# Kernel tuning notes

Measured on AMD Instinct MI355X. Metric: run time of the kernel, lower is better.

The kernel has to match this reference:

```python
import jax, jax.numpy as jnp
import numpy as np

NX, NY, NT = 128, 128, 64          # global space-time grid
LX, LY = 2.0, 2.0                  # periodic domain extents
K_NB = 128                         # neighbors per query
NHEAD = 4
EPS = 1e-5


def setup_inputs() -> dict:
    key = jax.random.key(0)
    ks = jax.random.split(key, 12)
    N = NX * NY * NT
    B, d, dff, L = 2048, 64, 128, 2
    nrm = lambda k, s: jax.random.normal(k, s, jnp.float32) * 0.05
    return {
        "q_lin_idx": jax.random.randint(ks[0], (B,), 0, N),
        "offsets_ijk": jax.random.randint(ks[1], (K_NB, 3), 0, 8),
        "coords": jax.random.uniform(ks[2], (N, 3), jnp.float32) * 2.0,
        "vals": jax.random.normal(ks[3], (N, 3), jnp.float32),
        "log_gammas": jnp.zeros((3,), jnp.float32),
        "proj_w": nrm(ks[4], (d, 6)), "proj_b": jnp.zeros((d,), jnp.float32),
        "qkv_w": nrm(ks[5], (L, 3 * d, d)), "qkv_b": jnp.zeros((L, 3 * d), jnp.float32),
        "out_w": nrm(ks[6], (L, d, d)), "out_b": jnp.zeros((L, d), jnp.float32),
        "ln1_s": jnp.ones((L, d), jnp.float32), "ln1_b": jnp.zeros((L, d), jnp.float32),
        "ff1_w": nrm(ks[7], (L, dff, d)), "ff1_b": jnp.zeros((L, dff), jnp.float32),
        "ff2_w": nrm(ks[8], (L, d, dff)), "ff2_b": jnp.zeros((L, d), jnp.float32),
        "ln2_s": jnp.ones((L, d), jnp.float32), "ln2_b": jnp.zeros((L, d), jnp.float32),
        "head_ln_s": jnp.ones((d,), jnp.float32), "head_ln_b": jnp.zeros((d,), jnp.float32),
        "head1_w": nrm(ks[9], (d, d)), "head1_b": jnp.zeros((d,), jnp.float32),
        "head2_w": nrm(ks[10], (3, d)), "head2_b": jnp.zeros((3,), jnp.float32),
    }


def _ln(x, s, b):
    m = x.mean(-1, keepdims=True)
    v = ((x - m) ** 2).mean(-1, keepdims=True)
    return (x - m) * jax.lax.rsqrt(v + EPS) * s + b


def _dper(a, b, L):
    # periodic relative delta in [-L/2, L/2)
    return (a - b + 0.5 * L) % L - 0.5 * L


def reference(q_lin_idx, offsets_ijk, coords, vals, log_gammas, proj_w, proj_b,
              qkv_w, qkv_b, out_w, out_b, ln1_s, ln1_b, ff1_w, ff1_b, ff2_w, ff2_b,
              ln2_s, ln2_b, head_ln_s, head_ln_b, head1_w, head1_b, head2_w, head2_b):
    # --- periodic-wrapped neighbor indices (div/mod on linear index) ---
    i = q_lin_idx // (NY * NT)
    r = q_lin_idx % (NY * NT)
    j = r // NT
    kk = r % NT
    di, dj, dk = offsets_ijk[:, 0], offsets_ijk[:, 1], offsets_ijk[:, 2]
    I = (i[:, None] + di[None, :]) % NX          # wrap_x
    J = (j[:, None] + dj[None, :]) % NY          # wrap_y
    T = jnp.clip(kk[:, None] + dk[None, :], 0, NT - 1)  # no wrap in t
    nb = I * (NY * NT) + J * NT + T              # [B, K]

    # --- gather + relative-delta encode ---
    q_xyz = coords[q_lin_idx]                    # [B, 3]
    nb_xyz = coords[nb]                          # [B, K, 3]
    dx = _dper(nb_xyz[..., 0], q_xyz[:, None, 0], LX)
    dy = _dper(nb_xyz[..., 1], q_xyz[:, None, 1], LY)
    dt = nb_xyz[..., 2] - q_xyz[:, None, 2]
    rel = jnp.stack([dx, dy, dt], -1) * jnp.exp(log_gammas)[None, None, :]
    tokens = jnp.concatenate([rel, vals[nb]], -1)  # [B, K, 6]

    # --- input projection + TransformerEncoder (post-norm, relu FF) ---
    h = tokens @ proj_w.T + proj_b               # [B, S, d]
    B, S, d = h.shape
    dh = d // NHEAD
    scale = 1.0 / np.sqrt(dh).astype(np.float32)
    for l in range(qkv_w.shape[0]):
        qkv = h @ qkv_w[l].T + qkv_b[l]
        qh, kh, vh = jnp.split(qkv, 3, axis=-1)
        qh = qh.reshape(B, S, NHEAD, dh).transpose(0, 2, 1, 3)
        kh = kh.reshape(B, S, NHEAD, dh).transpose(0, 2, 1, 3)
        vh = vh.reshape(B, S, NHEAD, dh).transpose(0, 2, 1, 3)
        att = jax.nn.softmax(jnp.einsum('bhqd,bhkd->bhqk', qh, kh) * scale, axis=-1)
        o = jnp.einsum('bhqk,bhkd->bhqd', att, vh).transpose(0, 2, 1, 3).reshape(B, S, d)
        h = _ln(h + (o @ out_w[l].T + out_b[l]), ln1_s[l], ln1_b[l])
        ff = jax.nn.relu(h @ ff1_w[l].T + ff1_b[l]) @ ff2_w[l].T + ff2_b[l]
        h = _ln(h + ff, ln2_s[l], ln2_b[l])

    # --- mean pool over neighbors + head ---
    hm = h.mean(axis=1)                          # [B, d]
    g = _ln(hm, head_ln_s, head_ln_b)
    g = jax.nn.gelu(g @ head1_w.T + head1_b, approximate=False)
    return g @ head2_w.T + head2_b               # [B, 3]
```

## Files before the change

### kernel.cpp

```cpp
#include <hip/hip_runtime.h>
#include <math.h>

#define NXg 128
#define NYg 128
#define NTg 64
#define SEQ 128
#define DIM 64
#define NH 4
#define DHd 16
#define DFFd 128
#define NLAYER 2
#define EPSf 1e-5f

typedef _Float16 f16x8 __attribute__((ext_vector_type(8)));
typedef _Float16 f16x4 __attribute__((ext_vector_type(4)));
typedef __fp16 fp16x2 __attribute__((ext_vector_type(2)));
typedef float f32x4 __attribute__((ext_vector_type(4)));

#define MFMA16(a, b, c) __builtin_amdgcn_mfma_f32_16x16x32_f16(a, b, c, 0, 0, 0)

union FragU { int d[4]; f16x8 v; };
union H4U  { int d[2]; f16x4 v; };
union P2U  { int i; fp16x2 h; };

__device__ __forceinline__ int pk2(float a, float b) {
  P2U u;
  u.h = __builtin_amdgcn_cvt_pkrtz(a, b);
  return u.i;
}
__device__ __forceinline__ float2 up2(int p) {
  P2U u; u.i = p;
  return make_float2((float)u.h[0], (float)u.h[1]);
}

__device__ __forceinline__ f16x8 zero8() {
  f16x8 z;
#pragma unroll
  for (int i = 0; i < 8; ++i) z[i] = (_Float16)0.0f;
  return z;
}
__device__ __forceinline__ f32x4 zero4f() {
  f32x4 z;
  z[0] = 0.f; z[1] = 0.f; z[2] = 0.f; z[3] = 0.f;
  return z;
}
__device__ __forceinline__ f16x8 ld8(const _Float16* p) { return *(const f16x8*)p; }

__device__ __forceinline__ f16x8 frag_k16p(int p0, int p1, int quad, int l15) {
  int slA = ((2 * quad) * 16 + l15) & 63;
  int slB = ((2 * quad + 1) * 16 + l15) & 63;
  FragU u;
  u.d[0] = __shfl(p0, slA, 64);
  u.d[1] = __shfl(p1, slA, 64);
  u.d[2] = __shfl(p0, slB, 64);
  u.d[3] = __shfl(p1, slB, 64);
  if (quad >= 2) { u.d[0] = 0; u.d[1] = 0; u.d[2] = 0; u.d[3] = 0; }
  return u.v;
}

__device__ __forceinline__ f16x8 frag_k64(const int* pk, int kt, int quad, int l15) {
  const int slA = (2 * (quad & 1)) * 16 + l15;
  const int slB = (2 * (quad & 1) + 1) * 16 + l15;
  const bool hi = quad >= 2;
  int a0 = __shfl(pk[4 * kt + 0], slA, 64), b0 = __shfl(pk[4 * kt + 2], slA, 64);
  int a1 = __shfl(pk[4 * kt + 1], slA, 64), b1 = __shfl(pk[4 * kt + 3], slA, 64);
  int a2 = __shfl(pk[4 * kt + 0], slB, 64), b2 = __shfl(pk[4 * kt + 2], slB, 64);
  int a3 = __shfl(pk[4 * kt + 1], slB, 64), b3 = __shfl(pk[4 * kt + 3], slB, 64);
  FragU u;
  u.d[0] = hi ? b0 : a0;
  u.d[1] = hi ? b1 : a1;
  u.d[2] = hi ? b2 : a2;
  u.d[3] = hi ? b3 : a3;
  return u.v;
}

__device__ __forceinline__ void res_ln_qt(const f32x4 acc[4], int pkX[8],
                                          const float* __restrict__ bias,
                                          const float* __restrict__ lns,
                                          const float* __restrict__ lnb,
                                          int quad) {
  float v[4][4];
  float s = 0.f;
#pragma unroll
  for (int mt = 0; mt < 4; ++mt) {
    f32x4 bb = *(const f32x4*)(bias + mt * 16 + quad * 4);
    float2 x0 = up2(pkX[mt * 2 + 0]);
    float2 x1 = up2(pkX[mt * 2 + 1]);
    v[mt][0] = acc[mt][0] + bb[0] + x0.x;
    v[mt][1] = acc[mt][1] + bb[1] + x0.y;
    v[mt][2] = acc[mt][2] + bb[2] + x1.x;
    v[mt][3] = acc[mt][3] + bb[3] + x1.y;
    s += (v[mt][0] + v[mt][1]) + (v[mt][2] + v[mt][3]);
  }
  s += __shfl_xor(s, 16, 64);
  s += __shfl_xor(s, 32, 64);
  const float mu = s * (1.0f / 64.0f);
  float q2 = 0.f;
#pragma unroll
  for (int mt = 0; mt < 4; ++mt)
#pragma unroll
    for (int jr = 0; jr < 4; ++jr) { float d = v[mt][jr] - mu; q2 = fmaf(d, d, q2); }
  q2 += __shfl_xor(q2, 16, 64);
  q2 += __shfl_xor(q2, 32, 64);
  const float rstd = rsqrtf(q2 * (1.0f / 64.0f) + EPSf);
#pragma unroll
  for (int mt = 0; mt < 4; ++mt) {
    f32x4 sv = *(const f32x4*)(lns + mt * 16 + quad * 4);
    f32x4 bv = *(const f32x4*)(lnb + mt * 16 + quad * 4);
    float o0 = fmaf((v[mt][0] - mu) * rstd, sv[0], bv[0]);
    float o1 = fmaf((v[mt][1] - mu) * rstd, sv[1], bv[1]);
    float o2 = fmaf((v[mt][2] - mu) * rstd, sv[2], bv[2]);
    float o3 = fmaf((v[mt][3] - mu) * rstd, sv[3], bv[3]);
    pkX[mt * 2 + 0] = pk2(o0, o1);
    pkX[mt * 2 + 1] = pk2(o2, o3);
  }
}

__global__ void prep_weights(const float* __restrict__ qkv_w,
                             const float* __restrict__ out_w,
                             const float* __restrict__ ff1_w,
                             const float* __restrict__ ff2_w,
                             _Float16* __restrict__ wsH) {
  int i = blockIdx.x * 256 + threadIdx.x;
  if (i < 24576) wsH[i] = (_Float16)qkv_w[i];
  else if (i < 32768) wsH[i] = (_Float16)out_w[i - 24576];
  else if (i < 49152) wsH[i] = (_Float16)ff1_w[i - 32768];
  else if (i < 65536) wsH[i] = (_Float16)ff2_w[i - 49152];
}

__global__ __launch_bounds__(256, 3)
void fieldformer_mfma(const int* __restrict__ q_lin_idx,
                      const int* __restrict__ offsets_ijk,
                      const float* __restrict__ coords,
                      const float* __restrict__ vals,
                      const float* __restrict__ log_gammas,
                      const float* __restrict__ proj_w,
                      const float* __restrict__ proj_b,
                      const float* __restrict__ qkv_b,
                      const float* __restrict__ out_b,
                      const float* __restrict__ ln1_s,
                      const float* __restrict__ ln1_b,
                      const float* __restrict__ ff1_b,
                      const float* __restrict__ ff2_b,
                      const float* __restrict__ ln2_s,
                      const float* __restrict__ ln2_b,
                      const float* __restrict__ head_ln_s,
                      const float* __restrict__ head_ln_b,
                      const float* __restrict__ head1_w,
                      const float* __restrict__ head1_b,
                      const float* __restrict__ head2_w,
                      const float* __restrict__ head2_b,
                      const _Float16* __restrict__ wH,
                      float* __restrict__ out) {
  __shared__ __align__(16) _Float16 sK[128 * 72];
  __shared__ __align__(16) _Float16 sV[64 * 136];

  const int tid = threadIdx.x;
  const int wv = tid >> 6;
  const int lane = tid & 63;
  const int quad = lane >> 4;
  const int l15 = lane & 15;
  const int b = blockIdx.x;

  {
    const int row = tid >> 1, hf = tid & 1;
    const int q = q_lin_idx[b];
    const int qi = q / (NYg * NTg);
    const int qrem = q - qi * (NYg * NTg);
    const int qj = qrem / NTg;
    const int qk = qrem - qj * NTg;
    const int di = offsets_ijk[row * 3 + 0];
    const int dj = offsets_ijk[row * 3 + 1];
    const int dk = offsets_ijk[row * 3 + 2];
    const int I = (qi + di) % NXg;
    const int J = (qj + dj) % NYg;
    int T = qk + dk; T = T < 0 ? 0 : (T > NTg - 1 ? NTg - 1 : T);
    const int nb = I * (NYg * NTg) + J * NTg + T;
    const float qx = coords[q * 3 + 0], qy = coords[q * 3 + 1], qz = coords[q * 3 + 2];
    const float nx_ = coords[nb * 3 + 0], ny_ = coords[nb * 3 + 1], nz_ = coords[nb * 3 + 2];
    float ax = nx_ - qx + 1.0f; ax -= 2.0f * floorf(ax * 0.5f); ax -= 1.0f;
    float ay = ny_ - qy + 1.0f; ay -= 2.0f * floorf(ay * 0.5f); ay -= 1.0f;
    const float at = nz_ - qz;
    float tok[6];
    tok[0] = ax * expf(log_gammas[0]);
    tok[1] = ay * expf(log_gammas[1]);
    tok[2] = at * expf(log_gammas[2]);
    tok[3] = vals[nb * 3 + 0];
    tok[4] = vals[nb * 3 + 1];
    tok[5] = vals[nb * 3 + 2];
#pragma unroll
    for (int ci = 0; ci < 32; ++ci) {
      const int c = hf * 32 + ci;
      const float* w = proj_w + c * 6;
      float a = proj_b[c];
      a = fmaf(tok[0], w[0], a); a = fmaf(tok[1], w[1], a);
      a = fmaf(tok[2], w[2], a); a = fmaf(tok[3], w[3], a);
      a = fmaf(tok[4], w[4], a); a = fmaf(tok[5], w[5], a);
      sK[row * 72 + c] = (_Float16)a;
    }
  }
  __syncthreads();

  int pkX[2][8];
#pragma unroll
  for (int qt = 0; qt < 2; ++qt) {
    const int q = (wv * 2 + qt) * 16 + l15;
#pragma unroll
    for (int mt = 0; mt < 4; ++mt) {
      int2 t = *(const int2*)(sK + q * 72 + mt * 16 + quad * 4);
      pkX[qt][mt * 2 + 0] = t.x;
      pkX[qt][mt * 2 + 1] = t.y;
    }
  }

  for (int l = 0; l < NLAYER; ++l) {
    const _Float16* qkvH = wH + l * 192 * 64;
    const _Float16* woutH = wH + 24576 + l * 64 * 64;
    const _Float16* ff1H = wH + 32768 + l * 128 * 64;
    const _Float16* ff2H = wH + 49152 + l * 64 * 128;
    const float* bqkv = qkv_b + l * 192;

    __syncthreads();

    int pkQ[2][8];
    {
      f16x8 bxf[2][2];
#pragma unroll
      for (int qt = 0; qt < 2; ++qt)
#pragma unroll
        for (int kt = 0; kt < 2; ++kt) bxf[qt][kt] = frag_k64(pkX[qt], kt, quad, l15);
#pragma unroll
      for (int hd = 0; hd < NH; ++hd) {
        f32x4 dq[2] = {zero4f(), zero4f()};
        f32x4 dk[2] = {zero4f(), zero4f()};
        f32x4 dv[2] = {zero4f(), zero4f()};
#pragma unroll
        for (int kt = 0; kt < 2; ++kt) {
          f16x8 awq = ld8(qkvH + (hd * 16 + l15) * 64 + kt * 32 + quad * 8);
          f16x8 awk = ld8(qkvH + (64 + hd * 16 + l15) * 64 + kt * 32 + quad * 8);
          f16x8 awv = ld8(qkvH + (128 + hd * 16 + l15) * 64 + kt * 32 + quad * 8);
#pragma unroll
          for (int qt = 0; qt < 2; ++qt) {
            dq[qt] = MFMA16(awq, bxf[qt][kt], dq[qt]);
            dk[qt] = MFMA16(awk, bxf[qt][kt], dk[qt]);
            dv[qt] = MFMA16(awv, bxf[qt][kt], dv[qt]);
          }
        }
        const f32x4 bq4 = *(const f32x4*)(bqkv + hd * 16 + quad * 4);
        const f32x4 bk4 = *(const f32x4*)(bqkv + 64 + hd * 16 + quad * 4);
        const f32x4 bv4 = *(const f32x4*)(bqkv + 128 + hd * 16 + quad * 4);
#pragma unroll
        for (int qt = 0; qt < 2; ++qt) {
          const int q = (wv * 2 + qt) * 16 + l15;
          H4U k4;
          k4.d[0] = pk2(dk[qt][0] + bk4[0], dk[qt][1] + bk4[1]);
          k4.d[1] = pk2(dk[qt][2] + bk4[2], dk[qt][3] + bk4[3]);
          *(f16x4*)(sK + q * 72 + hd * 16 + quad * 4) = k4.v;
#pragma unroll
          for (int jr = 0; jr < 4; ++jr)
            sV[(hd * 16 + quad * 4 + jr) * 136 + q] = (_Float16)(dv[qt][jr] + bv4[jr]);
          pkQ[qt][hd * 2 + 0] = pk2((dq[qt][0] + bq4[0]) * 0.25f, (dq[qt][1] + bq4[1]) * 0.25f);
          pkQ[qt][hd * 2 + 1] = pk2((dq[qt][2] + bq4[2]) * 0.25f, (dq[qt][3] + bq4[3]) * 0.25f);
        }
      }
    }
    __syncthreads();

    int pkO[2][8];
#pragma unroll
    for (int hd = 0; hd < NH; ++hd) {
#pragma unroll
      for (int qt = 0; qt < 2; ++qt) {
        f16x8 bqf = frag_k16p(pkQ[qt][hd * 2 + 0], pkQ[qt][hd * 2 + 1], quad, l15);
        float s0 = 0.f;
        f32x4 ov = zero4f();
#pragma unroll
        for (int kt2 = 0; kt2 < 4; ++kt2) {
          int pkP[4];
#pragma unroll
          for (int mi = 0; mi < 2; ++mi) {
            const int mt = kt2 * 2 + mi;
            f16x8 ak = (quad < 2) ? ld8(sK + (mt * 16 + l15) * 72 + hd * 16 + quad * 8)
                                  : zero8();
            f32x4 zc = zero4f();
            f32x4 sc = MFMA16(ak, bqf, zc);
            float e0 = __expf(sc[0]), e1 = __expf(sc[1]);
            float e2 = __expf(sc[2]), e3 = __expf(sc[3]);
            s0 += (e0 + e1) + (e2 + e3);
            pkP[mi * 2 + 0] = pk2(e0, e1);
            pkP[mi * 2 + 1] = pk2(e2, e3);
          }
          f16x8 av = ld8(sV + (hd * 16 + l15) * 136 + kt2 * 32 + quad * 8);
          f16x8 bp = frag_k64(pkP, 0, quad, l15);
          ov = MFMA16(av, bp, ov);
        }
        s0 += __shfl_xor(s0, 16, 64);
        s0 += __shfl_xor(s0, 32, 64);
        const float inv = 1.0f / s0;
        pkO[qt][hd * 2 + 0] = pk2(ov[0] * inv, ov[1] * inv);
        pkO[qt][hd * 2 + 1] = pk2(ov[2] * inv, ov[3] * inv);
      }
    }

#pragma unroll
    for (int qt = 0; qt < 2; ++qt) {
      f32x4 y2[4] = {zero4f(), zero4f(), zero4f(), zero4f()};
#pragma unroll
      for (int kt = 0; kt < 2; ++kt) {
        f16x8 bof = frag_k64(pkO[qt], kt, quad, l15);
#pragma unroll
        for (int mt = 0; mt < 4; ++mt) {
          f16x8 aw = ld8(woutH + (mt * 16 + l15) * 64 + kt * 32 + quad * 8);
          y2[mt] = MFMA16(aw, bof, y2[mt]);
        }
      }
      res_ln_qt(y2, pkX[qt], out_b + l * 64, ln1_s + l * 64, ln1_b + l * 64, quad);
    }

#pragma unroll
    for (int qt = 0; qt < 2; ++qt) {
      f16x8 bx2[2];
#pragma unroll
      for (int kt = 0; kt < 2; ++kt) bx2[kt] = frag_k64(pkX[qt], kt, quad, l15);
      const float* b1 = ff1_b + l * 128;
      f32x4 g4[4] = {zero4f(), zero4f(), zero4f(), zero4f()};
#pragma unroll
      for (int kt = 0; kt < 4; ++kt) {
        int pkH[4];
#pragma unroll
        for (int mi = 0; mi < 2; ++mi) {
          const int mt = kt * 2 + mi;
          f32x4 f8 = zero4f();
#pragma unroll
          for (int k2 = 0; k2 < 2; ++k2) {
            f16x8 aw = ld8(ff1H + (mt * 16 + l15) * 64 + k2 * 32 + quad * 8);
            f8 = MFMA16(aw, bx2[k2], f8);
          }
          f32x4 bb = *(const f32x4*)(b1 + mt * 16 + quad * 4);
          pkH[mi * 2 + 0] = pk2(fmaxf(f8[0] + bb[0], 0.f), fmaxf(f8[1] + bb[1], 0.f));
          pkH[mi * 2 + 1] = pk2(fmaxf(f8[2] + bb[2], 0.f), fmaxf(f8[3] + bb[3], 0.f));
        }
        f16x8 bh = frag_k64(pkH, 0, quad, l15);
#pragma unroll
        for (int mt2 = 0; mt2 < 4; ++mt2) {
          f16x8 aw = ld8(ff2H + (mt2 * 16 + l15) * 128 + kt * 32 + quad * 8);
          g4[mt2] = MFMA16(aw, bh, g4[mt2]);
        }
      }
      res_ln_qt(g4, pkX[qt], ff2_b + l * 64, ln2_s + l * 64, ln2_b + l * 64, quad);
    }
  }

  __syncthreads();
  {
    float* pf = (float*)sK;
    float* gsc = pf + 256;
    float* asc = gsc + 64;
    f32x4 cs[4];
#pragma unroll
    for (int mt = 0; mt < 4; ++mt) {
      float2 a0 = up2(pkX[0][mt * 2 + 0]), a1 = up2(pkX[0][mt * 2 + 1]);
      float2 b0 = up2(pkX[1][mt * 2 + 0]), b1 = up2(pkX[1][mt * 2 + 1]);
      cs[mt][0] = a0.x + b0.x;
      cs[mt][1] = a0.y + b0.y;
      cs[mt][2] = a1.x + b1.x;
      cs[mt][3] = a1.y + b1.y;
    }
#pragma unroll
    for (int d = 1; d <= 8; d <<= 1)
#pragma unroll
      for (int mt = 0; mt < 4; ++mt)
#pragma unroll
        for (int jr = 0; jr < 4; ++jr) cs[mt][jr] += __shfl_xor(cs[mt][jr], d, 64);
    if (l15 == 0) {
#pragma unroll
      for (int mt = 0; mt < 4; ++mt)
        *(f32x4*)(pf + wv * 64 + mt * 16 + quad * 4) = cs[mt];
    }
    __syncthreads();
    if (tid < 64) {
      const float hm = (pf[tid] + pf[64 + tid] + pf[128 + tid] + pf[192 + tid]) * (1.0f / 128.0f);
      float t = hm;
      t += __shfl_xor(t, 1, 64);  t += __shfl_xor(t, 2, 64);
      t += __shfl_xor(t, 4, 64);  t += __shfl_xor(t, 8, 64);
      t += __shfl_xor(t, 16, 64); t += __shfl_xor(t, 32, 64);
      const float mu = t * (1.0f / 64.0f);
      const float dv = hm - mu;
      float v2 = dv * dv;
      v2 += __shfl_xor(v2, 1, 64);  v2 += __shfl_xor(v2, 2, 64);
      v2 += __shfl_xor(v2, 4, 64);  v2 += __shfl_xor(v2, 8, 64);
      v2 += __shfl_xor(v2, 16, 64); v2 += __shfl_xor(v2, 32, 64);
      const float var = v2 * (1.0f / 64.0f);
      gsc[tid] = fmaf(dv * rsqrtf(var + EPSf), head_ln_s[tid], head_ln_b[tid]);
    }
    __syncthreads();
    if (tid < 64) {
      float z = head1_b[tid];
      for (int k = 0; k < 64; ++k) z = fmaf(gsc[k], head1_w[tid * 64 + k], z);
      asc[tid] = 0.5f * z * (1.0f + erff(z * 0.70710678118654752f));
    }
    __syncthreads();
    if (tid < 3) {
      float z = head2_b[tid];
      for (int k = 0; k < 64; ++k) z = fmaf(asc[k], head2_w[tid * 64 + k], z);
      out[b * 3 + tid] = z;
    }
  }
}

extern "C" void kernel_launch(void* const* d_in, const int* in_sizes, int n_in,
                              void* d_out, int out_size, void* d_ws, size_t ws_size,
                              hipStream_t stream) {
  (void)n_in; (void)ws_size; (void)out_size;
  const int B = in_sizes[0];
  _Float16* wsH = (_Float16*)d_ws;

  prep_weights<<<dim3(256), dim3(256), 0, stream>>>(
      (const float*)d_in[7],
      (const float*)d_in[9],
      (const float*)d_in[13],
      (const float*)d_in[15],
      wsH);

  fieldformer_mfma<<<dim3(B), dim3(256), 0, stream>>>(
      (const int*)d_in[0],
      (const int*)d_in[1],
      (const float*)d_in[2],
      (const float*)d_in[3],
      (const float*)d_in[4],
      (const float*)d_in[5],
      (const float*)d_in[6],
      (const float*)d_in[8],
      (const float*)d_in[10],
      (const float*)d_in[11],
      (const float*)d_in[12],
      (const float*)d_in[14],
      (const float*)d_in[16],
      (const float*)d_in[17],
      (const float*)d_in[18],
      (const float*)d_in[19],
      (const float*)d_in[20],
      (const float*)d_in[21],
      (const float*)d_in[22],
      (const float*)d_in[23],
      (const float*)d_in[24],
      wsH,
      (float*)d_out);
}
```

Baseline: 319.7 us.

## Use 512 threads per block with one 16-token tile per wave

Doubles the block to 8 waves so that each wave handles a single 16-row query tile instead of two, and the token projection is split four ways per row. This removes the per-wave qt loop, which cuts register pressure and raises the number of waves available to hide MFMA and LDS latency. The cost is that each wave now loads the shared weight fragments for only one tile, so weight-load reuse across tiles drops, and the final reduction sums over 8 per-wave partials.

```diff
diff --git a/kernel.cpp b/kernel.cpp
--- a/kernel.cpp
+++ b/kernel.cpp
@@ -128,7 +128,7 @@
   else if (i < 65536) wsH[i] = (_Float16)ff2_w[i - 49152];
 }
 
-__global__ __launch_bounds__(256, 3)
+__global__ __launch_bounds__(512, 4)
 void fieldformer_mfma(const int* __restrict__ q_lin_idx,
                       const int* __restrict__ offsets_ijk,
                       const float* __restrict__ coords,
@@ -161,12 +161,13 @@
   const int quad = lane >> 4;
   const int l15 = lane & 15;
   const int b = blockIdx.x;
+  const int q = wv * 16 + l15;
 
   {
-    const int row = tid >> 1, hf = tid & 1;
-    const int q = q_lin_idx[b];
-    const int qi = q / (NYg * NTg);
-    const int qrem = q - qi * (NYg * NTg);
+    const int row = tid >> 2, part = tid & 3;
+    const int qq = q_lin_idx[b];
+    const int qi = qq / (NYg * NTg);
+    const int qrem = qq - qi * (NYg * NTg);
     const int qj = qrem / NTg;
     const int qk = qrem - qj * NTg;
     const int di = offsets_ijk[row * 3 + 0];
@@ -176,7 +177,7 @@
     const int J = (qj + dj) % NYg;
     int T = qk + dk; T = T < 0 ? 0 : (T > NTg - 1 ? NTg - 1 : T);
     const int nb = I * (NYg * NTg) + J * NTg + T;
-    const float qx = coords[q * 3 + 0], qy = coords[q * 3 + 1], qz = coords[q * 3 + 2];
+    const float qx = coords[qq * 3 + 0], qy = coords[qq * 3 + 1], qz = coords[qq * 3 + 2];
     const float nx_ = coords[nb * 3 + 0], ny_ = coords[nb * 3 + 1], nz_ = coords[nb * 3 + 2];
     float ax = nx_ - qx + 1.0f; ax -= 2.0f * floorf(ax * 0.5f); ax -= 1.0f;
     float ay = ny_ - qy + 1.0f; ay -= 2.0f * floorf(ay * 0.5f); ay -= 1.0f;
@@ -189,8 +190,8 @@
     tok[4] = vals[nb * 3 + 1];
     tok[5] = vals[nb * 3 + 2];
 #pragma unroll
-    for (int ci = 0; ci < 32; ++ci) {
-      const int c = hf * 32 + ci;
+    for (int ci = 0; ci < 16; ++ci) {
+      const int c = part * 16 + ci;
       const float* w = proj_w + c * 6;
       float a = proj_b[c];
       a = fmaf(tok[0], w[0], a); a = fmaf(tok[1], w[1], a);
@@ -201,16 +202,12 @@
   }
   __syncthreads();
 
-  int pkX[2][8];
-#pragma unroll
-  for (int qt = 0; qt < 2; ++qt) {
-    const int q = (wv * 2 + qt) * 16 + l15;
-#pragma unroll
-    for (int mt = 0; mt < 4; ++mt) {
-      int2 t = *(const int2*)(sK + q * 72 + mt * 16 + quad * 4);
-      pkX[qt][mt * 2 + 0] = t.x;
-      pkX[qt][mt * 2 + 1] = t.y;
-    }
+  int pkX[8];
+#pragma unroll
+  for (int mt = 0; mt < 4; ++mt) {
+    int2 t = *(const int2*)(sK + q * 72 + mt * 16 + quad * 4);
+    pkX[mt * 2 + 0] = t.x;
+    pkX[mt * 2 + 1] = t.y;
   }
 
   for (int l = 0; l < NLAYER; ++l) {
@@ -222,106 +219,90 @@
 
     __syncthreads();
 
-    int pkQ[2][8];
+    int pkQ[8];
     {
-      f16x8 bxf[2][2];
-#pragma unroll
-      for (int qt = 0; qt < 2; ++qt)
-#pragma unroll
-        for (int kt = 0; kt < 2; ++kt) bxf[qt][kt] = frag_k64(pkX[qt], kt, quad, l15);
+      f16x8 bxf[2];
+#pragma unroll
+      for (int kt = 0; kt < 2; ++kt) bxf[kt] = frag_k64(pkX, kt, quad, l15);
 #pragma unroll
       for (int hd = 0; hd < NH; ++hd) {
-        f32x4 dq[2] = {zero4f(), zero4f()};
-        f32x4 dk[2] = {zero4f(), zero4f()};
-        f32x4 dv[2] = {zero4f(), zero4f()};
+        f32x4 dq = zero4f(), dk = zero4f(), dv = zero4f();
 #pragma unroll
         for (int kt = 0; kt < 2; ++kt) {
           f16x8 awq = ld8(qkvH + (hd * 16 + l15) * 64 + kt * 32 + quad * 8);
           f16x8 awk = ld8(qkvH + (64 + hd * 16 + l15) * 64 + kt * 32 + quad * 8);
           f16x8 awv = ld8(qkvH + (128 + hd * 16 + l15) * 64 + kt * 32 + quad * 8);
-#pragma unroll
-          for (int qt = 0; qt < 2; ++qt) {
-            dq[qt] = MFMA16(awq, bxf[qt][kt], dq[qt]);
-            dk[qt] = MFMA16(awk, bxf[qt][kt], dk[qt]);
-            dv[qt] = MFMA16(awv, bxf[qt][kt], dv[qt]);
-          }
+          dq = MFMA16(awq, bxf[kt], dq);
+          dk = MFMA16(awk, bxf[kt], dk);
+          dv = MFMA16(awv, bxf[kt], dv);
         }
         const f32x4 bq4 = *(const f32x4*)(bqkv + hd * 16 + quad * 4);
         const f32x4 bk4 = *(const f32x4*)(bqkv + 64 + hd * 16 + quad * 4);
         const f32x4 bv4 = *(const f32x4*)(bqkv + 128 + hd * 16 + quad * 4);
-#pragma unroll
-        for (int qt = 0; qt < 2; ++qt) {
-          const int q = (wv * 2 + qt) * 16 + l15;
-          H4U k4;
-          k4.d[0] = pk2(dk[qt][0] + bk4[0], dk[qt][1] + bk4[1]);
-          k4.d[1] = pk2(dk[qt][2] + bk4[2], dk[qt][3] + bk4[3]);
-          *(f16x4*)(sK + q * 72 + hd * 16 + quad * 4) = k4.v;
-#pragma unroll
-          for (int jr = 0; jr < 4; ++jr)
-            sV[(hd * 16 + quad * 4 + jr) * 136 + q] = (_Float16)(dv[qt][jr] + bv4[jr]);
-          pkQ[qt][hd * 2 + 0] = pk2((dq[qt][0] + bq4[0]) * 0.25f, (dq[qt][1] + bq4[1]) * 0.25f);
-          pkQ[qt][hd * 2 + 1] = pk2((dq[qt][2] + bq4[2]) * 0.25f, (dq[qt][3] + bq4[3]) * 0.25f);
+        H4U k4;
+        k4.d[0] = pk2(dk[0] + bk4[0], dk[1] + bk4[1]);
+        k4.d[1] = pk2(dk[2] + bk4[2], dk[3] + bk4[3]);
+        *(f16x4*)(sK + q * 72 + hd * 16 + quad * 4) = k4.v;
+#pragma unroll
+        for (int jr = 0; jr < 4; ++jr)
+          sV[(hd * 16 + quad * 4 + jr) * 136 + q] = (_Float16)(dv[jr] + bv4[jr]);
+        pkQ[hd * 2 + 0] = pk2((dq[0] + bq4[0]) * 0.25f, (dq[1] + bq4[1]) * 0.25f);
+        pkQ[hd * 2 + 1] = pk2((dq[2] + bq4[2]) * 0.25f, (dq[3] + bq4[3]) * 0.25f);
+      }
+    }
+    __syncthreads();
+
+    int pkO[8];
+#pragma unroll
+    for (int hd = 0; hd < NH; ++hd) {
+      f16x8 bqf = frag_k16p(pkQ[hd * 2 + 0], pkQ[hd * 2 + 1], quad, l15);
+      float s0 = 0.f;
+      f32x4 ov = zero4f();
+#pragma unroll
+      for (int kt2 = 0; kt2 < 4; ++kt2) {
+        int pkP[4];
+#pragma unroll
+        for (int mi = 0; mi < 2; ++mi) {
+          const int mt = kt2 * 2 + mi;
+          f16x8 ak = (quad < 2) ? ld8(sK + (mt * 16 + l15) * 72 + hd * 16 + quad * 8)
+                                : zero8();
+          f32x4 zc = zero4f();
+          f32x4 sc = MFMA16(ak, bqf, zc);
+          float e0 = __expf(sc[0]), e1 = __expf(sc[1]);
+          float e2 = __expf(sc[2]), e3 = __expf(sc[3]);
+          s0 += (e0 + e1) + (e2 + e3);
+          pkP[mi * 2 + 0] = pk2(e0, e1);
+          pkP[mi * 2 + 1] = pk2(e2, e3);
         }
+        f16x8 av = ld8(sV + (hd * 16 + l15) * 136 + kt2 * 32 + quad * 8);
+        f16x8 bp = frag_k64(pkP, 0, quad, l15);
+        ov = MFMA16(av, bp, ov);
       }
-    }
-    __syncthreads();
-
-    int pkO[2][8];
-#pragma unroll
-    for (int hd = 0; hd < NH; ++hd) {
-#pragma unroll
-      for (int qt = 0; qt < 2; ++qt) {
-        f16x8 bqf = frag_k16p(pkQ[qt][hd * 2 + 0], pkQ[qt][hd * 2 + 1], quad, l15);
-        float s0 = 0.f;
-        f32x4 ov = zero4f();
-#pragma unroll
-        for (int kt2 = 0; kt2 < 4; ++kt2) {
-          int pkP[4];
-#pragma unroll
-          for (int mi = 0; mi < 2; ++mi) {
-            const int mt = kt2 * 2 + mi;
-            f16x8 ak = (quad < 2) ? ld8(sK + (mt * 16 + l15) * 72 + hd * 16 + quad * 8)
-                                  : zero8();
-            f32x4 zc = zero4f();
-            f32x4 sc = MFMA16(ak, bqf, zc);
-            float e0 = __expf(sc[0]), e1 = __expf(sc[1]);
-            float e2 = __expf(sc[2]), e3 = __expf(sc[3]);
-            s0 += (e0 + e1) + (e2 + e3);
-            pkP[mi * 2 + 0] = pk2(e0, e1);
-            pkP[mi * 2 + 1] = pk2(e2, e3);
-          }
-          f16x8 av = ld8(sV + (hd * 16 + l15) * 136 + kt2 * 32 + quad * 8);
-          f16x8 bp = frag_k64(pkP, 0, quad, l15);
-          ov = MFMA16(av, bp, ov);
-        }
-        s0 += __shfl_xor(s0, 16, 64);
-        s0 += __shfl_xor(s0, 32, 64);
-        const float inv = 1.0f / s0;
-        pkO[qt][hd * 2 + 0] = pk2(ov[0] * inv, ov[1] * inv);
-        pkO[qt][hd * 2 + 1] = pk2(ov[2] * inv, ov[3] * inv);
-      }
-    }
-
-#pragma unroll
-    for (int qt = 0; qt < 2; ++qt) {
+      s0 += __shfl_xor(s0, 16, 64);
+      s0 += __shfl_xor(s0, 32, 64);
+      const float inv = 1.0f / s0;
+      pkO[hd * 2 + 0] = pk2(ov[0] * inv, ov[1] * inv);
+      pkO[hd * 2 + 1] = pk2(ov[2] * inv, ov[3] * inv);
+    }
+
+    {
       f32x4 y2[4] = {zero4f(), zero4f(), zero4f(), zero4f()};
 #pragma unroll
       for (int kt = 0; kt < 2; ++kt) {
-        f16x8 bof = frag_k64(pkO[qt], kt, quad, l15);
+        f16x8 bof = frag_k64(pkO, kt, quad, l15);
 #pragma unroll
         for (int mt = 0; mt < 4; ++mt) {
           f16x8 aw = ld8(woutH + (mt * 16 + l15) * 64 + kt * 32 + quad * 8);
           y2[mt] = MFMA16(aw, bof, y2[mt]);
         }
       }
-      res_ln_qt(y2, pkX[qt], out_b + l * 64, ln1_s + l * 64, ln1_b + l * 64, quad);
-    }
-
-#pragma unroll
-    for (int qt = 0; qt < 2; ++qt) {
+      res_ln_qt(y2, pkX, out_b + l * 64, ln1_s + l * 64, ln1_b + l * 64, quad);
+    }
+
+    {
       f16x8 bx2[2];
 #pragma unroll
-      for (int kt = 0; kt < 2; ++kt) bx2[kt] = frag_k64(pkX[qt], kt, quad, l15);
+      for (int kt = 0; kt < 2; ++kt) bx2[kt] = frag_k64(pkX, kt, quad, l15);
       const float* b1 = ff1_b + l * 128;
       f32x4 g4[4] = {zero4f(), zero4f(), zero4f(), zero4f()};
 #pragma unroll
@@ -347,24 +328,21 @@
           g4[mt2] = MFMA16(aw, bh, g4[mt2]);
         }
       }
-      res_ln_qt(g4, pkX[qt], ff2_b + l * 64, ln2_s + l * 64, ln2_b + l * 64, quad);
+      res_ln_qt(g4, pkX, ff2_b + l * 64, ln2_s + l * 64, ln2_b + l * 64, quad);
     }
   }
 
   __syncthreads();
   {
     float* pf = (float*)sK;
-    float* gsc = pf + 256;
+    float* gsc = pf + 512;
     float* asc = gsc + 64;
     f32x4 cs[4];
 #pragma unroll
     for (int mt = 0; mt < 4; ++mt) {
-      float2 a0 = up2(pkX[0][mt * 2 + 0]), a1 = up2(pkX[0][mt * 2 + 1]);
-      float2 b0 = up2(pkX[1][mt * 2 + 0]), b1 = up2(pkX[1][mt * 2 + 1]);
-      cs[mt][0] = a0.x + b0.x;
-      cs[mt][1] = a0.y + b0.y;
-      cs[mt][2] = a1.x + b1.x;
-      cs[mt][3] = a1.y + b1.y;
+      float2 x0 = up2(pkX[mt * 2 + 0]);
+      float2 x1 = up2(pkX[mt * 2 + 1]);
+      cs[mt][0] = x0.x; cs[mt][1] = x0.y; cs[mt][2] = x1.x; cs[mt][3] = x1.y;
     }
 #pragma unroll
     for (int d = 1; d <= 8; d <<= 1)
@@ -379,7 +357,10 @@
     }
     __syncthreads();
     if (tid < 64) {
-      const float hm = (pf[tid] + pf[64 + tid] + pf[128 + tid] + pf[192 + tid]) * (1.0f / 128.0f);
+      float hm = 0.f;
+#pragma unroll
+      for (int w = 0; w < 8; ++w) hm += pf[w * 64 + tid];
+      hm *= (1.0f / 128.0f);
       float t = hm;
       t += __shfl_xor(t, 1, 64);  t += __shfl_xor(t, 2, 64);
       t += __shfl_xor(t, 4, 64);  t += __shfl_xor(t, 8, 64);
@@ -422,7 +403,7 @@
       (const float*)d_in[15],
       wsH);
 
-  fieldformer_mfma<<<dim3(B), dim3(256), 0, stream>>>(
+  fieldformer_mfma<<<dim3(B), dim3(512), 0, stream>>>(
       (const int*)d_in[0],
       (const int*)d_in[1],
       (const float*)d_in[2],
```

Result: slower. 448.6 us (+40.3%).
